# Kernel optimization log

Hardware: AMD Instinct MI355X
Metric: run time of the kernel (lower is better)

## Reference

```python
import jax, jax.numpy as jnp
import numpy as np

B, N, C = 64, 8192, 64
C4 = C // 4
EPS_BN = 1e-5


def setup_inputs() -> dict:
    key = jax.random.key(0)
    ks = jax.random.split(key, 12)
    s = 0.05
    return {
        "x": jax.random.normal(ks[0], (B, N, 10), jnp.float32),
        "y": jax.random.normal(ks[1], (B, N, 13), jnp.float32),
        "W_l": jax.random.normal(ks[2], (10, C), jnp.float32) * s,
        "b_l": jax.random.normal(ks[3], (C,), jnp.float32) * s,
        "W_r": jax.random.normal(ks[4], (13, C), jnp.float32) * s,
        "b_r": jax.random.normal(ks[5], (C,), jnp.float32) * s,
        "W_qk": jax.random.normal(ks[6], (C4, C), jnp.float32) * s,  # shared q/k 1x1-conv weight
        "W_v": jax.random.normal(ks[7], (C, C), jnp.float32) * s,
        "b_v": jax.random.normal(ks[8], (C,), jnp.float32) * s,
        "W_t": jax.random.normal(ks[9], (C, C), jnp.float32) * s,
        "b_t": jax.random.normal(ks[10], (C,), jnp.float32) * s,
        "gamma": jnp.ones((C,), jnp.float32),
        "beta": jnp.zeros((C,), jnp.float32),
    }


def reference(x, y, W_l, b_l, W_r, b_r, W_qk, W_v, b_v, W_t, b_t, gamma, beta):
    # x: [B,N,10] -> linear_l; y: [B,N,13] -> linear_r  (torch keeps [B,C,N]; we keep [B,N,C])
    X = x @ W_l + b_l                                   # [B,N,C]
    Y = y @ W_r + b_r                                   # [B,N,C]
    # 1x1 convs == per-point matmuls; attention runs ACROSS the batch dim per point n
    xq = jnp.einsum('bnc,dc->nbd', X, W_qk)             # [N,B,C/4]
    yk = jnp.einsum('bnc,dc->nbd', Y, W_qk)             # [N,B,C/4] (shared weight)
    yv = jnp.einsum('bnc,dc->nbd', Y, W_v) + b_v        # [N,B,C]
    energy = jnp.einsum('nbd,ned->nbe', xq, yk)         # [N,B,B]
    attn = jax.nn.softmax(energy, axis=-1)
    # extra L1 renormalization over dim=1 (offset-attention style)
    attn = attn / (1e-9 + attn.sum(axis=1, keepdims=True))
    yr = jnp.einsum('nbe,nec->bnc', attn, yv)           # [B,N,C]
    # trans_conv -> BatchNorm (training-mode batch stats) -> ReLU -> residual -> max over points
    t = jnp.einsum('bnc,dc->bnd', X - yr, W_t) + b_t    # [B,N,C]
    mean = t.mean(axis=(0, 1))
    var = t.var(axis=(0, 1))                            # biased var, as BN uses
    tn = gamma * (t - mean) * jax.lax.rsqrt(var + EPS_BN) + beta
    xres = X + jax.nn.relu(tn)                          # [B,N,C]
    return jnp.max(xres, axis=1)[:, :, None]            # [B,C,1] to match torch layout
```

## Files before the change

kernel.cpp:

```cpp
#include <hip/hip_runtime.h>

#define B_ 64
#define N_ 8192

using short8 = __attribute__((ext_vector_type(8))) short;
using f32x4  = __attribute__((ext_vector_type(4))) float;

#define MFMA16(a, b, c) __builtin_amdgcn_mfma_f32_16x16x32_bf16((a), (b), (c), 0, 0, 0)

__device__ inline unsigned short f2bf(float f) {
  union { float f; unsigned int u; } v; v.f = f;
  return (unsigned short)((v.u + 0x8000u) >> 16);
}
__device__ inline float bf2f(unsigned int hi16_in_low) {
  union { unsigned int u; float f; } v; v.u = hi16_in_low << 16;
  return v.f;
}


__global__ void k0_prep(const float* __restrict__ W_l, const float* __restrict__ b_l,
                        const float* __restrict__ W_r, const float* __restrict__ b_r,
                        const float* __restrict__ W_qk, const float* __restrict__ W_v,
                        const float* __restrict__ b_v, const float* __restrict__ W_t,
                        float* __restrict__ wsf) {
  const int tid = threadIdx.x;
  unsigned short* wb   = (unsigned short*)(wsf + 66688);
  unsigned short* BM   = wb;
  unsigned short* BL   = wb + 512;
  unsigned short* BRV2 = wb + 2560;
  unsigned short* BT   = wb + 4608;
  if (blockIdx.x == 0) {
    __shared__ float Wlq[11 * 16], Wrk[14 * 16];
    for (int idx = tid; idx < 11 * 16; idx += 256) {
      int i = idx >> 4, d = idx & 15;
      const float* a = (i < 10) ? (W_l + i * 64) : b_l;
      float s = 0.f;
      for (int c = 0; c < 64; ++c) s = fmaf(a[c], W_qk[d * 64 + c], s);
      Wlq[idx] = s;
    }
    for (int idx = tid; idx < 14 * 16; idx += 256) {
      int j = idx >> 4, d = idx & 15;
      const float* a = (j < 13) ? (W_r + j * 64) : b_r;
      float s = 0.f;
      for (int c = 0; c < 64; ++c) s = fmaf(a[c], W_qk[d * 64 + c], s);
      Wrk[idx] = s;
    }
    __syncthreads();
    for (int idx = tid; idx < 512; idx += 256) {
      int j = idx >> 5, kk = idx & 31;
      unsigned short o = 0;
      if (j < 14 && kk < 11) {
        float s = 0.f;
        for (int d = 0; d < 16; ++d) s = fmaf(Wlq[kk * 16 + d], Wrk[j * 16 + d], s);
        o = f2bf(s);
      }
      BM[idx] = o;
    }
  } else if (blockIdx.x == 1) {
    for (int idx = tid; idx < 2048; idx += 256) {
      int c = idx >> 5, kk = idx & 31;
      unsigned short o = 0;
      if (kk < 13) {
        float s = 0.f;
        for (int j = 0; j < 64; ++j) s = fmaf(W_r[kk * 64 + j], W_v[c * 64 + j], s);
        o = f2bf(s);
      } else if (kk == 13) {
        float s = b_v[c];
        for (int j = 0; j < 64; ++j) s = fmaf(b_r[j], W_v[c * 64 + j], s);
        o = f2bf(s);
      }
      BRV2[idx] = o;
    }
  } else if (blockIdx.x == 2) {
    for (int idx = tid; idx < 2048; idx += 256) {
      int c = idx >> 5, kk = idx & 31;
      unsigned short o = 0;
      if (kk < 10) o = f2bf(W_l[kk * 64 + c]);
      else if (kk == 10) o = f2bf(b_l[c]);
      BL[idx] = o;
    }
    for (int i = tid; i < 1024; i += 256) wsf[i] = 0.f;
  } else {
    for (int i = tid; i < 4096; i += 256) BT[i] = f2bf(W_t[i]);
  }
}

__global__ __launch_bounds__(256, 3)
void k1_attn(const float* __restrict__ x, const float* __restrict__ y,
             const float* __restrict__ wsf, const float* __restrict__ b_t,
             float* __restrict__ stats) {
  __shared__ __align__(16) short lds[18688];
  __shared__ float scr[1024];
  short* const Axy[2] = {lds, lds + 2560};
  short* const YTb[2] = {lds + 5120, lds + 6272};
  short* const awB    = lds + 7424;
  short* const guB    = lds + 16640;

  const unsigned short* wb   = (const unsigned short*)(wsf + 66688);
  const unsigned short* BM   = wb;
  const unsigned short* BL   = wb + 512;
  const unsigned short* BRV2 = wb + 2560;
  const unsigned short* BT   = wb + 4608;
  unsigned short* tg = (unsigned short*)(wsf + 66688) + 8704;

  const int tid  = threadIdx.x;
  const int w    = tid >> 6;
  const int lane = tid & 63;
  const int l15  = lane & 15;
  const int q    = lane >> 4;
  const int r0   = w * 16;
  const int n0   = blockIdx.x * 2;
  short* const aw[2] = {awB + w * 1152, awB + (4 + w) * 1152};
  short* const gu[2] = {guB + w * 256,  guB + (4 + w) * 256};

  {
    const int b = tid >> 2, i = tid & 3;
#pragma unroll
    for (int p = 0; p < 2; ++p) {
      const float* xp = x + ((size_t)b * N_ + n0 + p) * 10;
      const float* yp = y + ((size_t)b * N_ + n0 + p) * 13;
      short* Ar = Axy[p] + b * 40;
      Ar[i]     = (short)f2bf(xp[i]);
      Ar[i + 4] = (short)f2bf(xp[i + 4]);
      short v8 = 0;
      if (i < 2) v8 = (short)f2bf(xp[i + 8]);
      else if (i == 2) v8 = (short)0x3F80;
      Ar[i + 8]  = v8;
      Ar[i + 12] = 0;
      const short y0 = (short)f2bf(yp[i]);
      const short y1 = (short)f2bf(yp[i + 4]);
      const short y2 = (short)f2bf(yp[i + 8]);
      short y3 = 0;
      if (i == 0) y3 = (short)f2bf(yp[12]);
      else if (i == 1) y3 = (short)0x3F80;
      Ar[16 + i] = y0;  Ar[20 + i] = y1;  Ar[24 + i] = y2;  Ar[28 + i] = y3;
      short* YT = YTb[p];
      YT[i * 72 + b] = y0;  YT[(i + 4) * 72 + b] = y1;
      YT[(i + 8) * 72 + b] = y2;  YT[(i + 12) * 72 + b] = y3;
    }
  }
  __syncthreads();

  const short8 z8 = {0, 0, 0, 0, 0, 0, 0, 0};
  const f32x4 zero4 = {0.f, 0.f, 0.f, 0.f};

  const short8 bmF = *(const short8*)&BM[l15 * 32 + q * 8];
  short8 blF[4];
#pragma unroll
  for (int f = 0; f < 4; ++f) blF[f] = *(const short8*)&BL[(f * 16 + l15) * 32 + q * 8];

  f32x4 X[2][4];
#pragma unroll
  for (int p = 0; p < 2; ++p) {
    const short8 aA = *(const short8*)&Axy[p][(r0 + l15) * 40 + q * 8];
    f32x4 G = MFMA16(aA, bmF, zero4);
#pragma unroll
    for (int f = 0; f < 4; ++f) X[p][f] = MFMA16(aA, blF[f], zero4);
#pragma unroll
    for (int j = 0; j < 4; ++j) gu[p][(q * 4 + j) * 16 + l15] = (short)f2bf(G[j]);
  }

  f32x4 E[2][4];
#pragma unroll
  for (int p = 0; p < 2; ++p) {
    short8 aG = z8;
    if (q < 2) aG = *(const short8*)&gu[p][l15 * 16 + q * 8];
#pragma unroll
    for (int f = 0; f < 4; ++f) {
      short8 bk = z8;
      if (q < 2) bk = *(const short8*)&Axy[p][(f * 16 + l15) * 40 + 16 + q * 8];
      E[p][f] = MFMA16(aG, bk, zero4);
    }
  }

  float inv_r[2][4];
#pragma unroll
  for (int p = 0; p < 2; ++p)
#pragma unroll
    for (int j = 0; j < 4; ++j) {
      float s = 0.f;
#pragma unroll
      for (int f = 0; f < 4; ++f) { E[p][f][j] = __expf(E[p][f][j]); s += E[p][f][j]; }
      s += __shfl_xor(s, 1);
      s += __shfl_xor(s, 2);
      s += __shfl_xor(s, 4);
      s += __shfl_xor(s, 8);
      inv_r[p][j] = 1.0f / s;
    }
#pragma unroll
  for (int p = 0; p < 2; ++p)
#pragma unroll
    for (int f = 0; f < 4; ++f) {
      float cs = E[p][f][0] * inv_r[p][0] + E[p][f][1] * inv_r[p][1] +
                 E[p][f][2] * inv_r[p][2] + E[p][f][3] * inv_r[p][3];
      cs += __shfl_xor(cs, 16);
      cs += __shfl_xor(cs, 32);
      if (lane < 16) scr[p * 256 + w * 64 + f * 16 + l15] = cs;
    }
  __syncthreads();

#pragma unroll
  for (int p = 0; p < 2; ++p) {
#pragma unroll
    for (int f = 0; f < 4; ++f) {
      const int col = f * 16 + l15;
      const float* sp = scr + p * 256;
      const float csv = 1.0f / (1e-9f + sp[col] + sp[64 + col] + sp[128 + col] + sp[192 + col]);
#pragma unroll
      for (int j = 0; j < 4; ++j)
        aw[p][(q * 4 + j) * 72 + col] = (short)f2bf(E[p][f][j] * inv_r[p][j] * csv);
    }
  }

  short8 brvF[4];
#pragma unroll
  for (int f = 0; f < 4; ++f) brvF[f] = *(const short8*)&BRV2[(f * 16 + l15) * 32 + q * 8];
#pragma unroll
  for (int p = 0; p < 2; ++p) {
    const short8 aA0 = *(const short8*)&aw[p][l15 * 72 + q * 8];
    const short8 aA1 = *(const short8*)&aw[p][l15 * 72 + 32 + q * 8];
    f32x4 U = MFMA16(aA0, *(const short8*)&YTb[p][l15 * 72 + q * 8], zero4);
    U = MFMA16(aA1, *(const short8*)&YTb[p][l15 * 72 + 32 + q * 8], U);
#pragma unroll
    for (int j = 0; j < 4; ++j) gu[p][(q * 4 + j) * 16 + l15] = (short)f2bf(U[j]);
    short8 aU = z8;
    if (q < 2) aU = *(const short8*)&gu[p][l15 * 16 + q * 8];
#pragma unroll
    for (int f = 0; f < 4; ++f) {
      f32x4 yr = MFMA16(aU, brvF[f], zero4);
#pragma unroll
      for (int j = 0; j < 4; ++j)
        aw[p][(q * 4 + j) * 72 + f * 16 + l15] = (short)f2bf(X[p][f][j] - yr[j]);
    }
  }

  f32x4 t[2][4];
  float sRed[2][4], ssRed[2][4];
#pragma unroll
  for (int p = 0; p < 2; ++p) {
    const short8 aZ0 = *(const short8*)&aw[p][l15 * 72 + q * 8];
    const short8 aZ1 = *(const short8*)&aw[p][l15 * 72 + 32 + q * 8];
#pragma unroll
    for (int f = 0; f < 4; ++f) {
      const int c = f * 16 + l15;
      const float bT = b_t[c];
      t[p][f] = MFMA16(aZ0, *(const short8*)&BT[c * 64 + q * 8], ((f32x4){bT, bT, bT, bT}));
      t[p][f] = MFMA16(aZ1, *(const short8*)&BT[c * 64 + 32 + q * 8], t[p][f]);
      float s = 0.f, ss = 0.f;
#pragma unroll
      for (int j = 0; j < 4; ++j) { s += t[p][f][j]; ss = fmaf(t[p][f][j], t[p][f][j], ss); }
      s  += __shfl_xor(s, 16);  s  += __shfl_xor(s, 32);
      ss += __shfl_xor(ss, 16); ss += __shfl_xor(ss, 32);
      sRed[p][f] = s; ssRed[p][f] = ss;
    }
  }
  __syncthreads();
#pragma unroll
  for (int p = 0; p < 2; ++p)
#pragma unroll
    for (int f = 0; f < 4; ++f)
      if (lane < 16) {
        scr[p * 512 + w * 64 + f * 16 + l15]       = sRed[p][f];
        scr[p * 512 + 256 + w * 64 + f * 16 + l15] = ssRed[p][f];
      }
  __syncthreads();
  if (tid < 128) {
    const int p = tid >> 6, c = tid & 63;
    const float* sp = scr + p * 512;
    const float s  = sp[c] + sp[64 + c] + sp[128 + c] + sp[192 + c];
    const float ss = sp[256 + c] + sp[320 + c] + sp[384 + c] + sp[448 + c];
    float* st = stats + ((n0 + p) & 7) * 128;
    atomicAdd(&st[c], s);
    atomicAdd(&st[64 + c], ss);
  }
#pragma unroll
  for (int p = 0; p < 2; ++p)
#pragma unroll
    for (int f = 0; f < 4; ++f)
#pragma unroll
      for (int j = 0; j < 4; ++j)
        tg[(size_t)(r0 + q * 4 + j) * (N_ * 64) + (size_t)(n0 + p) * 64 + f * 16 + l15] =
            f2bf(t[p][f][j]);
}

__global__ void k2_stats(const float* __restrict__ stats, float* __restrict__ meanr) {
  const int c = threadIdx.x;
  if (c < 64) {
    float s = 0.f, ss = 0.f;
    for (int r = 0; r < 8; ++r) { s += stats[r * 128 + c]; ss += stats[r * 128 + 64 + c]; }
    const float inv = 1.0f / (float)(B_ * N_);
    const float mu = s * inv;
    const float var = fmaf(ss, inv, -mu * mu);
    meanr[c] = mu;
    meanr[64 + c] = rsqrtf(var + 1e-5f);
  }
}

__global__ __launch_bounds__(256)
void k3_max(const float* __restrict__ x, const float* __restrict__ W_l,
            const float* __restrict__ b_l, const float* __restrict__ gamma,
            const float* __restrict__ beta, const unsigned short* __restrict__ tg,
            const float* __restrict__ meanr, float* __restrict__ pmax)
{
  const int b = blockIdx.x >> 4;
  const int chunk = blockIdx.x & 15;
  const int wv = threadIdx.x >> 6;
  const int lane = threadIdx.x & 63;
  const int c0 = (lane & 15) * 4;
  const int nsub = lane >> 4;
  float4 wl4[10];
#pragma unroll
  for (int k = 0; k < 10; ++k) wl4[k] = *(const float4*)&W_l[k * 64 + c0];
  const float4 bl  = *(const float4*)&b_l[c0];
  const float4 g   = *(const float4*)&gamma[c0];
  const float4 be  = *(const float4*)&beta[c0];
  const float4 mu  = *(const float4*)&meanr[c0];
  const float4 rs  = *(const float4*)&meanr[64 + c0];
  float4 grs, bmb;
  grs.x = g.x * rs.x; grs.y = g.y * rs.y; grs.z = g.z * rs.z; grs.w = g.w * rs.w;
  bmb.x = be.x - mu.x * grs.x; bmb.y = be.y - mu.y * grs.y;
  bmb.z = be.z - mu.z * grs.z; bmb.w = be.w - mu.w * grs.w;
  float4 m = {-1e30f, -1e30f, -1e30f, -1e30f};
  const size_t tgb = (size_t)b << 19;
  const int n0 = chunk * 512 + wv * 128 + nsub;
  for (int jj = 0; jj < 32; ++jj) {
    const int n = n0 + jj * 4;
    const uint2 tv = *(const uint2*)&tg[tgb + (size_t)n * 64 + c0];
    const float* xp = x + ((size_t)b * N_ + n) * 10;
    float4 X = bl;
#pragma unroll
    for (int k = 0; k < 10; ++k) {
      const float xk = xp[k];
      X.x = fmaf(xk, wl4[k].x, X.x); X.y = fmaf(xk, wl4[k].y, X.y);
      X.z = fmaf(xk, wl4[k].z, X.z); X.w = fmaf(xk, wl4[k].w, X.w);
    }
    const float t0 = bf2f(tv.x & 0xFFFFu), t1 = bf2f(tv.x >> 16);
    const float t2 = bf2f(tv.y & 0xFFFFu), t3 = bf2f(tv.y >> 16);
    m.x = fmaxf(m.x, X.x + fmaxf(fmaf(t0, grs.x, bmb.x), 0.f));
    m.y = fmaxf(m.y, X.y + fmaxf(fmaf(t1, grs.y, bmb.y), 0.f));
    m.z = fmaxf(m.z, X.z + fmaxf(fmaf(t2, grs.z, bmb.z), 0.f));
    m.w = fmaxf(m.w, X.w + fmaxf(fmaf(t3, grs.w, bmb.w), 0.f));
  }
  m.x = fmaxf(m.x, __shfl_xor(m.x, 16)); m.y = fmaxf(m.y, __shfl_xor(m.y, 16));
  m.z = fmaxf(m.z, __shfl_xor(m.z, 16)); m.w = fmaxf(m.w, __shfl_xor(m.w, 16));
  m.x = fmaxf(m.x, __shfl_xor(m.x, 32)); m.y = fmaxf(m.y, __shfl_xor(m.y, 32));
  m.z = fmaxf(m.z, __shfl_xor(m.z, 32)); m.w = fmaxf(m.w, __shfl_xor(m.w, 32));
  __shared__ float sm[4][64];
  if (lane < 16) *(float4*)&sm[wv][c0] = m;
  __syncthreads();
  if (threadIdx.x < 64) {
    const float r = fmaxf(fmaxf(sm[0][threadIdx.x], sm[1][threadIdx.x]),
                          fmaxf(sm[2][threadIdx.x], sm[3][threadIdx.x]));
    pmax[(size_t)blockIdx.x * 64 + threadIdx.x] = r;
  }
}

__global__ void k4_final(const float* __restrict__ pmax, float* __restrict__ out) {
  const int b = blockIdx.x, c = threadIdx.x;
  float m = -1e30f;
  for (int ch = 0; ch < 16; ++ch) m = fmaxf(m, pmax[((size_t)b * 16 + ch) * 64 + c]);
  out[b * 64 + c] = m;
}

extern "C" void kernel_launch(void* const* d_in, const int* in_sizes, int n_in,
                              void* d_out, int out_size, void* d_ws, size_t ws_size,
                              hipStream_t stream) {
  const float* x     = (const float*)d_in[0];
  const float* y     = (const float*)d_in[1];
  const float* W_l   = (const float*)d_in[2];
  const float* b_l   = (const float*)d_in[3];
  const float* W_r   = (const float*)d_in[4];
  const float* b_r   = (const float*)d_in[5];
  const float* W_qk  = (const float*)d_in[6];
  const float* W_v   = (const float*)d_in[7];
  const float* b_v   = (const float*)d_in[8];
  const float* W_t   = (const float*)d_in[9];
  const float* b_t   = (const float*)d_in[10];
  const float* gamma = (const float*)d_in[11];
  const float* beta  = (const float*)d_in[12];
  float* out = (float*)d_out;

  float* wsf = (float*)d_ws;
  float* stats = wsf;
  float* meanr = wsf + 1024;
  float* pmax  = wsf + 1152;
  const unsigned short* tg = (const unsigned short*)(wsf + 66688) + 8704;

  hipLaunchKernelGGL(k0_prep, dim3(4), dim3(256), 0, stream,
                     W_l, b_l, W_r, b_r, W_qk, W_v, b_v, W_t, wsf);
  hipLaunchKernelGGL(k1_attn, dim3(N_ / 2), dim3(256), 0, stream,
                     x, y, wsf, b_t, stats);
  hipLaunchKernelGGL(k2_stats, dim3(1), dim3(64), 0, stream, stats, meanr);
  hipLaunchKernelGGL(k3_max, dim3(1024), dim3(256), 0, stream,
                     x, W_l, b_l, gamma, beta, tg, meanr, pmax);
  hipLaunchKernelGGL(k4_final, dim3(64), dim3(64), 0, stream, pmax, out);
}
```

Before: 207.2 us.

## Cut attention kernel LDS and registers, fold stats and final max into k3

The attention kernel now reuses a single per-wave scratch buffer across both points instead of double buffers, shrinking LDS, and raises launch bounds from 3 to 5 blocks per SM. It drops the precomputed X and weight-fragment registers and instead recomputes X MFMAs late with weight fragments loaded on demand. The separate stats and final-max kernels are removed: every k3 block recomputes mean/rstd from stats, and the last block per batch does the final max reduction using an atomic counter. This saves two launches but adds redundant stats work and fence/atomic overhead, and may serialize the per-point phases.

```diff
diff --git a/kernel.cpp b/kernel.cpp
--- a/kernel.cpp
+++ b/kernel.cpp
@@ -24,7 +24,7 @@
                         const float* __restrict__ b_v, const float* __restrict__ W_t,
                         float* __restrict__ wsf) {
   const int tid = threadIdx.x;
-  unsigned short* wb   = (unsigned short*)(wsf + 66688);
+  unsigned short* wb   = (unsigned short*)(wsf + 66624);
   unsigned short* BM   = wb;
   unsigned short* BL   = wb + 512;
   unsigned short* BRV2 = wb + 2560;
@@ -79,29 +79,29 @@
       else if (kk == 10) o = f2bf(b_l[c]);
       BL[idx] = o;
     }
-    for (int i = tid; i < 1024; i += 256) wsf[i] = 0.f;
+    for (int i = tid; i < 1088; i += 256) wsf[i] = 0.f;
   } else {
     for (int i = tid; i < 4096; i += 256) BT[i] = f2bf(W_t[i]);
   }
 }
 
-__global__ __launch_bounds__(256, 3)
+__global__ __launch_bounds__(256, 5)
 void k1_attn(const float* __restrict__ x, const float* __restrict__ y,
              const float* __restrict__ wsf, const float* __restrict__ b_t,
              float* __restrict__ stats) {
-  __shared__ __align__(16) short lds[18688];
+  __shared__ __align__(16) short lds[13056];
   __shared__ float scr[1024];
   short* const Axy[2] = {lds, lds + 2560};
   short* const YTb[2] = {lds + 5120, lds + 6272};
   short* const awB    = lds + 7424;
-  short* const guB    = lds + 16640;
-
-  const unsigned short* wb   = (const unsigned short*)(wsf + 66688);
+  short* const guB    = lds + 12032;
+
+  const unsigned short* wb   = (const unsigned short*)(wsf + 66624);
   const unsigned short* BM   = wb;
   const unsigned short* BL   = wb + 512;
   const unsigned short* BRV2 = wb + 2560;
   const unsigned short* BT   = wb + 4608;
-  unsigned short* tg = (unsigned short*)(wsf + 66688) + 8704;
+  unsigned short* tg = (unsigned short*)(wsf + 66624) + 8704;
 
   const int tid  = threadIdx.x;
   const int w    = tid >> 6;
@@ -110,8 +110,8 @@
   const int q    = lane >> 4;
   const int r0   = w * 16;
   const int n0   = blockIdx.x * 2;
-  short* const aw[2] = {awB + w * 1152, awB + (4 + w) * 1152};
-  short* const gu[2] = {guB + w * 256,  guB + (4 + w) * 256};
+  short* const aw = awB + w * 1152;
+  short* const gu = guB + w * 256;
 
   {
     const int b = tid >> 2, i = tid & 3;
@@ -143,28 +143,18 @@
 
   const short8 z8 = {0, 0, 0, 0, 0, 0, 0, 0};
   const f32x4 zero4 = {0.f, 0.f, 0.f, 0.f};
-
   const short8 bmF = *(const short8*)&BM[l15 * 32 + q * 8];
-  short8 blF[4];
-#pragma unroll
-  for (int f = 0; f < 4; ++f) blF[f] = *(const short8*)&BL[(f * 16 + l15) * 32 + q * 8];
-
-  f32x4 X[2][4];
+
+  short8 aAp[2];
+  f32x4 E[2][4];
 #pragma unroll
   for (int p = 0; p < 2; ++p) {
-    const short8 aA = *(const short8*)&Axy[p][(r0 + l15) * 40 + q * 8];
-    f32x4 G = MFMA16(aA, bmF, zero4);
-#pragma unroll
-    for (int f = 0; f < 4; ++f) X[p][f] = MFMA16(aA, blF[f], zero4);
-#pragma unroll
-    for (int j = 0; j < 4; ++j) gu[p][(q * 4 + j) * 16 + l15] = (short)f2bf(G[j]);
-  }
-
-  f32x4 E[2][4];
-#pragma unroll
-  for (int p = 0; p < 2; ++p) {
+    aAp[p] = *(const short8*)&Axy[p][(r0 + l15) * 40 + q * 8];
+    f32x4 G = MFMA16(aAp[p], bmF, zero4);
+#pragma unroll
+    for (int j = 0; j < 4; ++j) gu[(q * 4 + j) * 16 + l15] = (short)f2bf(G[j]);
     short8 aG = z8;
-    if (q < 2) aG = *(const short8*)&gu[p][l15 * 16 + q * 8];
+    if (q < 2) aG = *(const short8*)&gu[l15 * 16 + q * 8];
 #pragma unroll
     for (int f = 0; f < 4; ++f) {
       short8 bk = z8;
@@ -173,7 +163,6 @@
     }
   }
 
-  float inv_r[2][4];
 #pragma unroll
   for (int p = 0; p < 2; ++p)
 #pragma unroll
@@ -185,20 +174,23 @@
       s += __shfl_xor(s, 2);
       s += __shfl_xor(s, 4);
       s += __shfl_xor(s, 8);
-      inv_r[p][j] = 1.0f / s;
+      const float inv = 1.0f / s;
+#pragma unroll
+      for (int f = 0; f < 4; ++f) E[p][f][j] *= inv;
     }
 #pragma unroll
   for (int p = 0; p < 2; ++p)
 #pragma unroll
     for (int f = 0; f < 4; ++f) {
-      float cs = E[p][f][0] * inv_r[p][0] + E[p][f][1] * inv_r[p][1] +
-                 E[p][f][2] * inv_r[p][2] + E[p][f][3] * inv_r[p][3];
+      float cs = E[p][f][0] + E[p][f][1] + E[p][f][2] + E[p][f][3];
       cs += __shfl_xor(cs, 16);
       cs += __shfl_xor(cs, 32);
       if (lane < 16) scr[p * 256 + w * 64 + f * 16 + l15] = cs;
     }
   __syncthreads();
 
+  f32x4 t[2][4];
+  float sRed[2][4], ssRed[2][4];
 #pragma unroll
   for (int p = 0; p < 2; ++p) {
 #pragma unroll
@@ -208,38 +200,27 @@
       const float csv = 1.0f / (1e-9f + sp[col] + sp[64 + col] + sp[128 + col] + sp[192 + col]);
 #pragma unroll
       for (int j = 0; j < 4; ++j)
-        aw[p][(q * 4 + j) * 72 + col] = (short)f2bf(E[p][f][j] * inv_r[p][j] * csv);
-    }
-  }
-
-  short8 brvF[4];
-#pragma unroll
-  for (int f = 0; f < 4; ++f) brvF[f] = *(const short8*)&BRV2[(f * 16 + l15) * 32 + q * 8];
-#pragma unroll
-  for (int p = 0; p < 2; ++p) {
-    const short8 aA0 = *(const short8*)&aw[p][l15 * 72 + q * 8];
-    const short8 aA1 = *(const short8*)&aw[p][l15 * 72 + 32 + q * 8];
+        aw[(q * 4 + j) * 72 + col] = (short)f2bf(E[p][f][j] * csv);
+    }
+    const short8 aA0 = *(const short8*)&aw[l15 * 72 + q * 8];
+    const short8 aA1 = *(const short8*)&aw[l15 * 72 + 32 + q * 8];
     f32x4 U = MFMA16(aA0, *(const short8*)&YTb[p][l15 * 72 + q * 8], zero4);
     U = MFMA16(aA1, *(const short8*)&YTb[p][l15 * 72 + 32 + q * 8], U);
 #pragma unroll
-    for (int j = 0; j < 4; ++j) gu[p][(q * 4 + j) * 16 + l15] = (short)f2bf(U[j]);
+    for (int j = 0; j < 4; ++j) gu[(q * 4 + j) * 16 + l15] = (short)f2bf(U[j]);
     short8 aU = z8;
-    if (q < 2) aU = *(const short8*)&gu[p][l15 * 16 + q * 8];
-#pragma unroll
-    for (int f = 0; f < 4; ++f) {
-      f32x4 yr = MFMA16(aU, brvF[f], zero4);
+    if (q < 2) aU = *(const short8*)&gu[l15 * 16 + q * 8];
+#pragma unroll
+    for (int f = 0; f < 4; ++f) {
+      const int c = f * 16 + l15;
+      f32x4 Xf = MFMA16(aAp[p], *(const short8*)&BL[c * 32 + q * 8], zero4);
+      f32x4 yr = MFMA16(aU, *(const short8*)&BRV2[c * 32 + q * 8], zero4);
 #pragma unroll
       for (int j = 0; j < 4; ++j)
-        aw[p][(q * 4 + j) * 72 + f * 16 + l15] = (short)f2bf(X[p][f][j] - yr[j]);
-    }
-  }
-
-  f32x4 t[2][4];
-  float sRed[2][4], ssRed[2][4];
-#pragma unroll
-  for (int p = 0; p < 2; ++p) {
-    const short8 aZ0 = *(const short8*)&aw[p][l15 * 72 + q * 8];
-    const short8 aZ1 = *(const short8*)&aw[p][l15 * 72 + 32 + q * 8];
+        aw[(q * 4 + j) * 72 + c] = (short)f2bf(Xf[j] - yr[j]);
+    }
+    const short8 aZ0 = *(const short8*)&aw[l15 * 72 + q * 8];
+    const short8 aZ1 = *(const short8*)&aw[l15 * 72 + 32 + q * 8];
 #pragma unroll
     for (int f = 0; f < 4; ++f) {
       const int c = f * 16 + l15;
@@ -283,29 +264,31 @@
             f2bf(t[p][f][j]);
 }
 
-__global__ void k2_stats(const float* __restrict__ stats, float* __restrict__ meanr) {
-  const int c = threadIdx.x;
-  if (c < 64) {
-    float s = 0.f, ss = 0.f;
-    for (int r = 0; r < 8; ++r) { s += stats[r * 128 + c]; ss += stats[r * 128 + 64 + c]; }
-    const float inv = 1.0f / (float)(B_ * N_);
-    const float mu = s * inv;
-    const float var = fmaf(ss, inv, -mu * mu);
-    meanr[c] = mu;
-    meanr[64 + c] = rsqrtf(var + 1e-5f);
-  }
-}
-
 __global__ __launch_bounds__(256)
 void k3_max(const float* __restrict__ x, const float* __restrict__ W_l,
             const float* __restrict__ b_l, const float* __restrict__ gamma,
             const float* __restrict__ beta, const unsigned short* __restrict__ tg,
-            const float* __restrict__ meanr, float* __restrict__ pmax)
+            const float* __restrict__ stats, float* __restrict__ pmax,
+            unsigned int* __restrict__ cnt, float* __restrict__ out)
 {
+  __shared__ float mrs[128];
+  __shared__ float sm[4][64];
+  __shared__ int lastFlag;
   const int b = blockIdx.x >> 4;
   const int chunk = blockIdx.x & 15;
-  const int wv = threadIdx.x >> 6;
-  const int lane = threadIdx.x & 63;
+  const int tid = threadIdx.x;
+  if (tid < 64) {
+    float s = 0.f, ss = 0.f;
+    for (int r = 0; r < 8; ++r) { s += stats[r * 128 + tid]; ss += stats[r * 128 + 64 + tid]; }
+    const float inv = 1.0f / (float)(B_ * N_);
+    const float mu = s * inv;
+    const float var = fmaf(ss, inv, -mu * mu);
+    mrs[tid] = mu;
+    mrs[64 + tid] = rsqrtf(var + 1e-5f);
+  }
+  __syncthreads();
+  const int wv = tid >> 6;
+  const int lane = tid & 63;
   const int c0 = (lane & 15) * 4;
   const int nsub = lane >> 4;
   float4 wl4[10];
@@ -314,8 +297,8 @@
   const float4 bl  = *(const float4*)&b_l[c0];
   const float4 g   = *(const float4*)&gamma[c0];
   const float4 be  = *(const float4*)&beta[c0];
-  const float4 mu  = *(const float4*)&meanr[c0];
-  const float4 rs  = *(const float4*)&meanr[64 + c0];
+  const float4 mu  = *(const float4*)&mrs[c0];
+  const float4 rs  = *(const float4*)&mrs[64 + c0];
   float4 grs, bmb;
   grs.x = g.x * rs.x; grs.y = g.y * rs.y; grs.z = g.z * rs.z; grs.w = g.w * rs.w;
   bmb.x = be.x - mu.x * grs.x; bmb.y = be.y - mu.y * grs.y;
@@ -323,6 +306,7 @@
   float4 m = {-1e30f, -1e30f, -1e30f, -1e30f};
   const size_t tgb = (size_t)b << 19;
   const int n0 = chunk * 512 + wv * 128 + nsub;
+#pragma unroll 4
   for (int jj = 0; jj < 32; ++jj) {
     const int n = n0 + jj * 4;
     const uint2 tv = *(const uint2*)&tg[tgb + (size_t)n * 64 + c0];
@@ -345,21 +329,28 @@
   m.z = fmaxf(m.z, __shfl_xor(m.z, 16)); m.w = fmaxf(m.w, __shfl_xor(m.w, 16));
   m.x = fmaxf(m.x, __shfl_xor(m.x, 32)); m.y = fmaxf(m.y, __shfl_xor(m.y, 32));
   m.z = fmaxf(m.z, __shfl_xor(m.z, 32)); m.w = fmaxf(m.w, __shfl_xor(m.w, 32));
-  __shared__ float sm[4][64];
   if (lane < 16) *(float4*)&sm[wv][c0] = m;
   __syncthreads();
-  if (threadIdx.x < 64) {
-    const float r = fmaxf(fmaxf(sm[0][threadIdx.x], sm[1][threadIdx.x]),
-                          fmaxf(sm[2][threadIdx.x], sm[3][threadIdx.x]));
-    pmax[(size_t)blockIdx.x * 64 + threadIdx.x] = r;
-  }
-}
-
-__global__ void k4_final(const float* __restrict__ pmax, float* __restrict__ out) {
-  const int b = blockIdx.x, c = threadIdx.x;
-  float m = -1e30f;
-  for (int ch = 0; ch < 16; ++ch) m = fmaxf(m, pmax[((size_t)b * 16 + ch) * 64 + c]);
-  out[b * 64 + c] = m;
+  if (tid < 64) {
+    const float r = fmaxf(fmaxf(sm[0][tid], sm[1][tid]), fmaxf(sm[2][tid], sm[3][tid]));
+    pmax[(size_t)blockIdx.x * 64 + tid] = r;
+  }
+  __threadfence();
+  __syncthreads();
+  if (tid == 0) {
+    const unsigned old = atomicAdd(&cnt[b], 1u);
+    lastFlag = (old == 15u);
+  }
+  __syncthreads();
+  if (lastFlag) {
+    __threadfence();
+    if (tid < 64) {
+      float r = -1e30f;
+      for (int ch = 0; ch < 16; ++ch)
+        r = fmaxf(r, pmax[(size_t)(b * 16 + ch) * 64 + tid]);
+      out[b * 64 + tid] = r;
+    }
+  }
 }
 
 extern "C" void kernel_launch(void* const* d_in, const int* in_sizes, int n_in,
@@ -382,16 +373,14 @@
 
   float* wsf = (float*)d_ws;
   float* stats = wsf;
-  float* meanr = wsf + 1024;
-  float* pmax  = wsf + 1152;
-  const unsigned short* tg = (const unsigned short*)(wsf + 66688) + 8704;
+  unsigned int* cnt = (unsigned int*)(wsf + 1024);
+  float* pmax  = wsf + 1088;
+  const unsigned short* tg = (const unsigned short*)(wsf + 66624) + 8704;
 
   hipLaunchKernelGGL(k0_prep, dim3(4), dim3(256), 0, stream,
                      W_l, b_l, W_r, b_r, W_qk, W_v, b_v, W_t, wsf);
   hipLaunchKernelGGL(k1_attn, dim3(N_ / 2), dim3(256), 0, stream,
                      x, y, wsf, b_t, stats);
-  hipLaunchKernelGGL(k2_stats, dim3(1), dim3(64), 0, stream, stats, meanr);
   hipLaunchKernelGGL(k3_max, dim3(1024), dim3(256), 0, stream,
-                     x, W_l, b_l, gamma, beta, tg, meanr, pmax);
-  hipLaunchKernelGGL(k4_final, dim3(64), dim3(64), 0, stream, pmax, out);
-}
+                     x, W_l, b_l, gamma, beta, tg, stats, pmax, cnt, out);
+}
```

New measurement: 332.7 us. 1.61x slower.
